# Kernel optimization log

Hardware: AMD Instinct MI355X
Metric: run time of the kernel (lower is better)

## Reference

```python
import jax, jax.numpy as jnp
from jax import lax
import numpy as np

# TopoLoss(dim=1, p=2, topo_lambda=1.0)
# p=2 -> Euclidean ground metric for the Vietoris-Rips filtration.
# This reference computes the dominant H0 persistence diagram of the VR complex:
# for a point cloud, H0 births are all 0 and deaths are exactly the MST edge
# weights (Kruskal/union-find == Prim, computed here with a fixed-length scan).
# Wasserstein distance between the two diagrams (equal cardinality N-1, births 0)
# reduces to optimal 1D matching of the sorted death values (q=1, the
# torch_topological WassersteinDistance default).
TOPO_LAMBDA = 1.0
EPS = 1e-12


def _pairwise_euclidean(x):
    # x: [B, N, D] -> [B, N, N] via the Gram trick (avoids [B,N,N,D] temp)
    sq = jnp.sum(x * x, axis=-1)                      # [B, N]
    g = jnp.einsum('bnd,bmd->bnm', x, x)              # [B, N, N]
    d2 = sq[:, :, None] + sq[:, None, :] - 2.0 * g
    return jnp.sqrt(jnp.maximum(d2, 0.0) + EPS)


def _mst_deaths(D):
    # Prim's algorithm on a dense distance matrix D: [N, N].
    # Returns the sorted MST edge weights = H0 death times ([N-1]).
    N = D.shape[0]
    inf = jnp.asarray(jnp.inf, D.dtype)
    in_tree0 = jnp.zeros((N,), bool).at[0].set(True)
    min_dist0 = D[0]

    def step(carry, _):
        in_tree, min_dist = carry
        masked = jnp.where(in_tree, inf, min_dist)
        j = jnp.argmin(masked)
        death = masked[j]
        in_tree = in_tree.at[j].set(True)
        min_dist = jnp.minimum(min_dist, D[j])
        return (in_tree, min_dist), death

    _, deaths = lax.scan(step, (in_tree0, min_dist0), None, length=N - 1)
    return jnp.sort(deaths)


def _h0_diagram_deaths(x):
    # x: [B, N, D] -> sorted death values [B, N-1]
    D = _pairwise_euclidean(x)
    return jax.vmap(_mst_deaths)(D)


def setup_inputs() -> dict:
    key = jax.random.key(0)
    k1, k2 = jax.random.split(key)
    B, N, D = 64, 1024, 3
    gts = jax.random.normal(k1, (B, N, D), dtype=jnp.float32)
    preds = jax.random.normal(k2, (B, N, D), dtype=jnp.float32)
    return {"gts": gts, "preds": preds}


def reference(gts, preds):
    # note: source names pers_info_pred = complex(gts) (vars swapped there);
    # Wasserstein is symmetric so ordering is irrelevant.
    deaths_a = _h0_diagram_deaths(gts)    # [B, N-1]
    deaths_b = _h0_diagram_deaths(preds)  # [B, N-1]
    # W1 between diagrams with equal cardinality and births==0:
    # optimal matching of sorted death coordinates.
    per_batch = jnp.sum(jnp.abs(deaths_a - deaths_b), axis=-1)  # [B]
    return per_batch.mean() * TOPO_LAMBDA
```

## Files before the change

### kernel.cpp

```cpp
#include <hip/hip_runtime.h>
#include <math.h>

#define N 1024
#define T 1024
#define HALF 512
#define PHASE_CAP 10
#define SWITCH 160

typedef float v2f __attribute__((ext_vector_type(2)));
typedef unsigned long long ull;

#define INF64 0xFFFFFFFFFFFFFFFFull
#define INF32 0xFFFFFFFFu

__device__ __forceinline__ unsigned umin32(unsigned a, unsigned b) { return a < b ? a : b; }
__device__ __forceinline__ unsigned umax32(unsigned a, unsigned b) { return a > b ? a : b; }
__device__ __forceinline__ int imin32(int a, int b) { return a < b ? a : b; }

__device__ __forceinline__ unsigned walk_root(const unsigned* parent, unsigned x) {
    unsigned prev = x, cur = parent[x];
    while (cur != prev) {
        unsigned nxt = parent[cur];
        if (nxt == prev) { cur = umin32(cur, prev); break; }
        prev = cur; cur = nxt;
    }
    return cur;
}

#define DPP_MIN_SHR(v, sh)                                                                   \
    do {                                                                                     \
        unsigned _t = (unsigned)__builtin_amdgcn_update_dpp(                                 \
            (int)0xFFFFFFFF, (int)(v), 0x110 | (sh), 0xF, 0xF, false);                       \
        (v) = umin32((v), _t);                                                               \
    } while (0)

__global__ __launch_bounds__(T) void scan1_kernel(const float* __restrict__ gts,
                                                  const float* __restrict__ preds,
                                                  unsigned* __restrict__ bests1) {
    __shared__ float px[N], py[N], pz[N];
    __shared__ float stage[3 * N];
    __shared__ unsigned pb[2][HALF];
    const int t = threadIdx.x;
    const int cloud = blockIdx.x >> 1;
    const int nh = blockIdx.x & 1;
    const float* __restrict__ src = (cloud < 64 ? gts : preds) + (size_t)(cloud & 63) * N * 3;

    if (t < 768) ((float4*)stage)[t] = ((const float4*)src)[t];
    __syncthreads();
    px[t] = stage[3 * t]; py[t] = stage[3 * t + 1]; pz[t] = stage[3 * t + 2];
    __syncthreads();

    const int node = nh * HALF + (t & (HALF - 1));
    const int jb = (t >> 9) * HALF;
    const float ax = px[node], ay = py[node], az = pz[node];
    const v2f axv = (v2f){ax, ax}, ayv = (v2f){ay, ay}, azv = (v2f){az, az};
    unsigned best = INF32;
    #pragma unroll 8
    for (int jj = 0; jj < HALF; jj += 2) {
        int j = jb + jj;
        v2f qx = *(const v2f*)&px[j];
        v2f qy = *(const v2f*)&py[j];
        v2f qz = *(const v2f*)&pz[j];
        v2f dx = axv - qx, dy = ayv - qy, dz = azv - qz;
        v2f e = dx * dx;
        e = __builtin_elementwise_fma(dy, dy, e);
        e = __builtin_elementwise_fma(dz, dz, e);
        unsigned k0 = (__float_as_uint(e.x) & 0xFFFFF800u) | (unsigned)j;
        unsigned k1 = (__float_as_uint(e.y) & 0xFFFFF800u) | (unsigned)(j + 1);
        k0 = (j == node) ? INF32 : k0;
        k1 = (j + 1 == node) ? INF32 : k1;
        best = umin32(best, umin32(k0, k1));
    }
    pb[t >> 9][t & (HALF - 1)] = best;
    __syncthreads();
    if (t < HALF)
        bests1[(size_t)cloud * N + nh * HALF + t] = umin32(pb[0][t], pb[1][t]);
}

__global__ __launch_bounds__(T) void scan2_kernel(const float* __restrict__ gts,
                                                  const float* __restrict__ preds,
                                                  const unsigned* __restrict__ bests1,
                                                  unsigned* __restrict__ bests2) {
    __shared__ float px[N], py[N], pz[N];
    __shared__ float stage[3 * N];
    __shared__ unsigned cw[N];
    __shared__ unsigned parent[N];
    __shared__ unsigned pb[2][HALF];
    const int t = threadIdx.x;
    const int cloud = blockIdx.x >> 1;
    const int nh = blockIdx.x & 1;
    const float* __restrict__ src = (cloud < 64 ? gts : preds) + (size_t)(cloud & 63) * N * 3;

    if (t < 768) ((float4*)stage)[t] = ((const float4*)src)[t];
    __syncthreads();
    px[t] = stage[3 * t]; py[t] = stage[3 * t + 1]; pz[t] = stage[3 * t + 2];
    parent[t] = bests1[(size_t)cloud * N + t] & 0x3FFu;
    __syncthreads();
    {
        unsigned r = walk_root(parent, (unsigned)t);
        parent[t] = r;
        cw[t] = r;
    }
    __syncthreads();

    const int node = nh * HALF + (t & (HALF - 1));
    const int jb = (t >> 9) * HALF;
    const unsigned c0 = cw[node];
    const float ax = px[node], ay = py[node], az = pz[node];
    const v2f axv = (v2f){ax, ax}, ayv = (v2f){ay, ay}, azv = (v2f){az, az};
    unsigned best = INF32;
    #pragma unroll 8
    for (int jj = 0; jj < HALF; jj += 2) {
        int j = jb + jj;
        v2f qx = *(const v2f*)&px[j];
        v2f qy = *(const v2f*)&py[j];
        v2f qz = *(const v2f*)&pz[j];
        uint2 cj = *(const uint2*)&cw[j];
        v2f dx = axv - qx, dy = ayv - qy, dz = azv - qz;
        v2f e = dx * dx;
        e = __builtin_elementwise_fma(dy, dy, e);
        e = __builtin_elementwise_fma(dz, dz, e);
        unsigned k0 = (__float_as_uint(e.x) & 0xFFFFF800u) | (unsigned)j;
        unsigned k1 = (__float_as_uint(e.y) & 0xFFFFF800u) | (unsigned)(j + 1);
        k0 = (cj.x == c0) ? INF32 : k0;
        k1 = (cj.y == c0) ? INF32 : k1;
        best = umin32(best, umin32(k0, k1));
    }
    pb[t >> 9][t & (HALF - 1)] = best;
    __syncthreads();
    if (t < HALF)
        bests2[(size_t)cloud * N + nh * HALF + t] = umin32(pb[0][t], pb[1][t]);
}

__global__ __launch_bounds__(T) void final_kernel(const float* __restrict__ gts,
                                                  const float* __restrict__ preds,
                                                  float* __restrict__ ws,
                                                  const unsigned* __restrict__ bests1,
                                                  const unsigned* __restrict__ bests2,
                                                  int nPre) {
    __shared__ float4 pts[N];
    __shared__ float4 spts[N];
    __shared__ unsigned comp[N];
    __shared__ ull bestComp[N];
    __shared__ unsigned parent[N];
    __shared__ __align__(16) unsigned pb[2][N];
    __shared__ float deaths[N];
    __shared__ int deathCount;

    const int t = threadIdx.x;
    const int blk = blockIdx.x;
    const float* __restrict__ src = (blk < 64 ? gts : preds) + (size_t)(blk & 63) * N * 3;

    {
        float* stg = (float*)&spts[0];
        if (t < 768) ((float4*)stg)[t] = ((const float4*)src)[t];
        __syncthreads();
        float x = stg[3 * t], y = stg[3 * t + 1], z = stg[3 * t + 2];
        pts[t] = make_float4(x, y, z, __uint_as_float((unsigned)t));
        comp[t] = (unsigned)t;
        parent[t] = (unsigned)t;
        deaths[t] = 0.0f;
        bestComp[t] = INF64;
    }
    if (t == 0) deathCount = 0;
    __syncthreads();

    const int n = t & (HALF - 1);
    const int h = t >> 9;
    const int n2 = n + HALF;
    const int jbase = h * HALF;
    float4 pA = pts[n], pB = pts[n2];
    const v2f pxv = (v2f){pA.x, pB.x};
    const v2f pyv = (v2f){pA.y, pB.y};
    const v2f pzv = (v2f){pA.z, pB.z};

    if (nPre >= 1) {
        unsigned b1 = bests1[(size_t)blk * N + t];
        unsigned j1 = b1 & 0x3FFu;
        unsigned e1 = b1 & 0xFFFFF800u;
        parent[t] = j1;
        __syncthreads();
        {
            unsigned p = j1;
            unsigned gp = parent[p];
            bool mutual = (gp == (unsigned)t);
            bool rec = !mutual || ((unsigned)t < p);
            float dval = rec ? sqrtf(__uint_as_float(e1) + 1e-12f) : 0.0f;
            ull m = __ballot(rec);
            int cnt = __popcll(m);
            int base = 0;
            if ((t & 63) == 0 && cnt) base = atomicAdd(&deathCount, cnt);
            base = __shfl(base, 0, 64);
            if (rec) {
                int idx = base + __popcll(m & ((1ull << (t & 63)) - 1ull));
                if (idx < N - 1) deaths[idx] = dval;
            }
        }
        __syncthreads();
        {
            unsigned r = walk_root(parent, (unsigned)t);
            parent[t] = r;
            comp[t] = r;
            pts[t].w = __uint_as_float(r);
        }
        __syncthreads();
    }

    if (nPre >= 2) {
        unsigned b2 = bests2[(size_t)blk * N + t];
        if (b2 != INF32) {
            unsigned j2 = b2 & 0x3FFu, e2 = b2 & 0xFFFFF800u;
            unsigned mn = umin32((unsigned)t, j2), mx = umax32((unsigned)t, j2);
            atomicMin(&bestComp[comp[t]], ((ull)e2 << 20) | (ull)((mn << 10) | mx));
        }
        __syncthreads();
        const unsigned c = (unsigned)t;
        const bool isRoot = (parent[c] == c);
        {
            ull bc = bestComp[c];
            if (isRoot && bc != INF64) {
                unsigned mn = (unsigned)((bc >> 10) & 0x3FFu);
                unsigned mx = (unsigned)(bc & 0x3FFu);
                unsigned cm = comp[mn];
                parent[c] = (cm == c) ? comp[mx] : cm;
            }
        }
        __syncthreads();
        {
            bool rec = false;
            float dval = 0.0f;
            unsigned p = parent[c];
            if (isRoot && p != c) {
                unsigned gp = parent[p];
                bool mutual = (gp == c);
                rec = !mutual || (c < p);
                if (rec) dval = sqrtf(__uint_as_float((unsigned)(bestComp[c] >> 20)) + 1e-12f);
            }
            ull m = __ballot(rec);
            int cnt = __popcll(m);
            int base = 0;
            if ((t & 63) == 0 && cnt) base = atomicAdd(&deathCount, cnt);
            base = __shfl(base, 0, 64);
            if (rec) {
                int idx = base + __popcll(m & ((1ull << (t & 63)) - 1ull));
                if (idx < N - 1) deaths[idx] = dval;
            }
        }
        __syncthreads();
        {
            unsigned r = walk_root(parent, c);
            parent[t] = r;
            unsigned nc = walk_root(parent, comp[t]);
            comp[t] = nc;
            pts[t].w = __uint_as_float(nc);
            bestComp[t] = INF64;
        }
        __syncthreads();
    }

    int phase = nPre;
    while (N - deathCount > SWITCH && phase < PHASE_CAP) {
        const unsigned c0 = comp[n], c1 = comp[n2];
        unsigned best0 = INF32, best1 = INF32;
        #pragma unroll 8
        for (int jj = 0; jj < HALF; ++jj) {
            int j = jbase + jj;
            float4 pj = pts[j];
            unsigned cj = __float_as_uint(pj.w);
            v2f dx = pxv - (v2f){pj.x, pj.x};
            v2f dy = pyv - (v2f){pj.y, pj.y};
            v2f dz = pzv - (v2f){pj.z, pj.z};
            v2f e = dx * dx;
            e = __builtin_elementwise_fma(dy, dy, e);
            e = __builtin_elementwise_fma(dz, dz, e);
            unsigned k0 = (__float_as_uint(e.x) & 0xFFFFF800u) | (unsigned)j;
            unsigned k1 = (__float_as_uint(e.y) & 0xFFFFF800u) | (unsigned)j;
            k0 = (cj == c0) ? INF32 : k0;
            k1 = (cj == c1) ? INF32 : k1;
            best0 = umin32(best0, k0);
            best1 = umin32(best1, k1);
        }
        pb[h][n] = best0;
        pb[h][n2] = best1;
        __syncthreads();
        if (h == 0) {
            #pragma unroll
            for (int s = 0; s < 2; ++s) {
                int m = s == 0 ? n : n2;
                unsigned fb = umin32(pb[0][m], pb[1][m]);
                if (fb != INF32) {
                    unsigned j = fb & 0x3FFu, e = fb & 0xFFFFF800u;
                    unsigned mn = umin32((unsigned)m, j), mx = umax32((unsigned)m, j);
                    ull key = ((ull)e << 20) | (ull)((mn << 10) | mx);
                    if (phase == 0) bestComp[m] = key;
                    else atomicMin(&bestComp[comp[m]], key);
                }
            }
        }
        __syncthreads();
        const unsigned c = (unsigned)t;
        const bool isRoot = (parent[c] == c);
        {
            ull bc = bestComp[c];
            if (isRoot && bc != INF64) {
                unsigned mn = (unsigned)((bc >> 10) & 0x3FFu);
                unsigned mx = (unsigned)(bc & 0x3FFu);
                unsigned cm = comp[mn];
                parent[c] = (cm == c) ? comp[mx] : cm;
            }
        }
        __syncthreads();
        {
            bool rec = false;
            float dval = 0.0f;
            unsigned p = parent[c];
            if (isRoot && p != c) {
                unsigned gp = parent[p];
                bool mutual = (gp == c);
                rec = !mutual || (c < p);
                if (rec) dval = sqrtf(__uint_as_float((unsigned)(bestComp[c] >> 20)) + 1e-12f);
            }
            ull m = __ballot(rec);
            int cnt = __popcll(m);
            int base = 0;
            if ((t & 63) == 0 && cnt) base = atomicAdd(&deathCount, cnt);
            base = __shfl(base, 0, 64);
            if (rec) {
                int idx = base + __popcll(m & ((1ull << (t & 63)) - 1ull));
                if (idx < N - 1) deaths[idx] = dval;
            }
        }
        __syncthreads();
        {
            unsigned r = walk_root(parent, c);
            parent[t] = r;
            unsigned nc = walk_root(parent, comp[t]);
            comp[t] = nc;
            pts[t].w = __uint_as_float(nc);
            bestComp[t] = INF64;
        }
        __syncthreads();
        ++phase;
    }

    const int dcbase = deathCount;
    const int comps = N - dcbase;
    if (comps > 1) {
        unsigned* sk = &pb[0][0];
        unsigned* wavemin = &pb[1][0];
        uint2* segs = (uint2*)&bestComp[0];
        sk[t] = (comp[t] << 10) | (unsigned)t;
        __syncthreads();
        for (int k = 2; k <= N; k <<= 1) {
            for (int j = k >> 1; j > 0; j >>= 1) {
                int ixj = t ^ j;
                if (ixj > t) {
                    unsigned a = sk[t], cc = sk[ixj];
                    bool up = ((t & k) == 0);
                    if ((a > cc) == up) { sk[t] = cc; sk[ixj] = a; }
                }
                __syncthreads();
            }
        }
        {
            unsigned key = sk[t];
            unsigned cme = key >> 10;
            spts[t] = pts[key & 0x3FFu];
            if (t == 0 || (sk[t - 1] >> 10) != cme) segs[cme].x = (unsigned)t;
            if (t == N - 1 || (sk[t + 1] >> 10) != cme) segs[cme].y = (unsigned)t + 1;
        }
        __syncthreads();

        const int lane = t & 63;
        const int wid = t >> 6;
        unsigned c_cur = comp[0];
        v2f pxv2 = (v2f){0.f, 0.f}, pyv2 = pxv2, pzv2 = pxv2;
        unsigned myc0 = 0, myc1 = 0, md0 = INF32, md1 = INF32;
        if (t < HALF) {
            float4 q0 = spts[t], q1 = spts[t + HALF];
            myc0 = sk[t] >> 10;
            myc1 = sk[t + HALF] >> 10;
            pxv2 = (v2f){q0.x, q1.x};
            pyv2 = (v2f){q0.y, q1.y};
            pzv2 = (v2f){q0.z, q1.z};
            if (myc0 == c_cur) pxv2.x = INFINITY;
            if (myc1 == c_cur) pxv2.y = INFINITY;
        }

        for (int step = 0; step < comps - 1; ++step) {
            if (t < HALF) {
                uint2 sg = segs[c_cur];
                const int jb = (int)sg.x, je = (int)sg.y, jl = je - 1;
                for (int base = jb; base < je; base += 4) {
                    float4 q0 = spts[base];
                    float4 q1 = spts[imin32(base + 1, jl)];
                    float4 q2 = spts[imin32(base + 2, jl)];
                    float4 q3 = spts[imin32(base + 3, jl)];
                    #define RELAX(qq)                                                        \
                        {                                                                    \
                            v2f dx = pxv2 - (v2f){qq.x, qq.x};                               \
                            v2f dy = pyv2 - (v2f){qq.y, qq.y};                               \
                            v2f dz = pzv2 - (v2f){qq.z, qq.z};                               \
                            v2f e = dx * dx;                                                 \
                            e = __builtin_elementwise_fma(dy, dy, e);                        \
                            e = __builtin_elementwise_fma(dz, dz, e);                        \
                            md0 = umin32(md0, (__float_as_uint(e.x) & 0xFFFFFC00u) | myc0);  \
                            md1 = umin32(md1, (__float_as_uint(e.y) & 0xFFFFFC00u) | myc1);  \
                        }
                    RELAX(q0) RELAX(q1) RELAX(q2) RELAX(q3)
                    #undef RELAX
                }
                unsigned v = umin32(md0, md1);
                DPP_MIN_SHR(v, 1);
                DPP_MIN_SHR(v, 2);
                DPP_MIN_SHR(v, 4);
                DPP_MIN_SHR(v, 8);
                unsigned r0 = (unsigned)__builtin_amdgcn_readlane((int)v, 15);
                unsigned r1 = (unsigned)__builtin_amdgcn_readlane((int)v, 31);
                unsigned r2 = (unsigned)__builtin_amdgcn_readlane((int)v, 47);
                unsigned r3 = (unsigned)__builtin_amdgcn_readlane((int)v, 63);
                if (lane == 0)
                    wavemin[(step & 1) * 8 + wid] = umin32(umin32(r0, r1), umin32(r2, r3));
            }
            __syncthreads();
            if (t < HALF) {
                const uint4* wmv = (const uint4*)(wavemin + (step & 1) * 8);
                uint4 u0 = wmv[0], u1 = wmv[1];
                unsigned m0 = umin32(umin32(u0.x, u0.y), umin32(u0.z, u0.w));
                unsigned m1 = umin32(umin32(u1.x, u1.y), umin32(u1.z, u1.w));
                unsigned G = umin32(m0, m1);
                c_cur = G & 0x3FFu;
                if (t == 0)
                    deaths[dcbase + step] = sqrtf(__uint_as_float(G & 0xFFFFFC00u) + 1e-12f);
                if (myc0 == c_cur) { pxv2.x = INFINITY; md0 = INF32; }
                if (myc1 == c_cur) { pxv2.y = INFINITY; md1 = INF32; }
            }
        }
    }

    if (t == 0) deaths[N - 1] = INFINITY;
    __syncthreads();
    for (int k = 2; k <= N; k <<= 1) {
        for (int j = k >> 1; j > 0; j >>= 1) {
            int ixj = t ^ j;
            if (ixj > t) {
                float a = deaths[t], cc = deaths[ixj];
                bool up = ((t & k) == 0);
                if ((a > cc) == up) { deaths[t] = cc; deaths[ixj] = a; }
            }
            __syncthreads();
        }
    }

    float* dst = ws + (size_t)blk * N;
    dst[t] = (t < N - 1) ? deaths[t] : 0.0f;
}

__global__ __launch_bounds__(256) void diff_kernel(const float* __restrict__ ws,
                                                   float* __restrict__ out) {
    __shared__ float red[4];
    const int t = threadIdx.x;
    const int b = blockIdx.x;
    const float* a = ws + (size_t)b * N;
    const float* c = ws + (size_t)(64 + b) * N;
    float sum = 0.0f;
    for (int i = t; i < N; i += 256)
        sum += fabsf(a[i] - c[i]);
    #pragma unroll
    for (int off = 32; off > 0; off >>= 1)
        sum += __shfl_down(sum, off, 64);
    if ((t & 63) == 0) red[t >> 6] = sum;
    __syncthreads();
    if (t == 0)
        atomicAdd(out, (red[0] + red[1] + red[2] + red[3]) * (1.0f / 64.0f));
}

extern "C" void kernel_launch(void* const* d_in, const int* in_sizes, int n_in,
                              void* d_out, int out_size, void* d_ws, size_t ws_size,
                              hipStream_t stream) {
    const float* gts = (const float*)d_in[0];
    const float* preds = (const float*)d_in[1];
    float* ws = (float*)d_ws;
    unsigned* bests1 = (unsigned*)d_ws;
    unsigned* bests2 = bests1 + 128 * N;
    const bool big = ws_size >= (size_t)(2u * 128u * N * 4u);

    if (big) {
        hipLaunchKernelGGL(scan1_kernel, dim3(256), dim3(T), 0, stream, gts, preds, bests1);
        hipLaunchKernelGGL(scan2_kernel, dim3(256), dim3(T), 0, stream, gts, preds, bests1, bests2);
        hipLaunchKernelGGL(final_kernel, dim3(128), dim3(T), 0, stream,
                           gts, preds, ws, bests1, bests2, 2);
    } else {
        hipLaunchKernelGGL(final_kernel, dim3(128), dim3(T), 0, stream,
                           gts, preds, ws, (const unsigned*)nullptr, (const unsigned*)nullptr, 0);
    }
    hipMemsetAsync(d_out, 0, sizeof(float), stream);
    hipLaunchKernelGGL(diff_kernel, dim3(64), dim3(256), 0, stream, ws, (float*)d_out);
}
```

Measured before the change: 233.4 us.

## Add third Boruvka prepass kernel to offload another phase from final kernel

Adds a scan3 kernel that rebuilds the component labels after phases one and two, then computes each node's nearest out-of-component neighbour over 256 blocks (two per cloud). The final kernel now loops over the precomputed phases, consuming bests3 as a third Boruvka merge step, which leaves fewer components for its own single-block-per-cloud search. It only runs when the workspace holds three buffers. In exchange it adds an extra kernel launch, a redundant recomputation of the earlier merges, and more global traffic.

```diff
diff --git a/kernel.cpp b/kernel.cpp
--- a/kernel.cpp
+++ b/kernel.cpp
@@ -132,11 +132,92 @@
         bests2[(size_t)cloud * N + nh * HALF + t] = umin32(pb[0][t], pb[1][t]);
 }
 
+__global__ __launch_bounds__(T) void scan3_kernel(const float* __restrict__ gts,
+                                                  const float* __restrict__ preds,
+                                                  const unsigned* __restrict__ bests1,
+                                                  const unsigned* __restrict__ bests2,
+                                                  unsigned* __restrict__ bests3) {
+    __shared__ float px[N], py[N], pz[N];
+    __shared__ float stage[3 * N];
+    __shared__ unsigned cw[N];
+    __shared__ unsigned parent[N];
+    __shared__ ull bestC[N];
+    __shared__ unsigned pb[2][HALF];
+    const int t = threadIdx.x;
+    const int cloud = blockIdx.x >> 1;
+    const int nh = blockIdx.x & 1;
+    const float* __restrict__ src = (cloud < 64 ? gts : preds) + (size_t)(cloud & 63) * N * 3;
+
+    if (t < 768) ((float4*)stage)[t] = ((const float4*)src)[t];
+    __syncthreads();
+    px[t] = stage[3 * t]; py[t] = stage[3 * t + 1]; pz[t] = stage[3 * t + 2];
+    parent[t] = bests1[(size_t)cloud * N + t] & 0x3FFu;
+    bestC[t] = INF64;
+    __syncthreads();
+    {
+        unsigned r = walk_root(parent, (unsigned)t);
+        parent[t] = r;
+        cw[t] = r;
+    }
+    __syncthreads();
+    {
+        unsigned b2 = bests2[(size_t)cloud * N + t];
+        if (b2 != INF32) {
+            unsigned j2 = b2 & 0x3FFu, e2 = b2 & 0xFFFFF800u;
+            unsigned mn = umin32((unsigned)t, j2), mx = umax32((unsigned)t, j2);
+            atomicMin(&bestC[cw[t]], ((ull)e2 << 20) | (ull)((mn << 10) | mx));
+        }
+    }
+    __syncthreads();
+    {
+        const unsigned c = (unsigned)t;
+        ull bc = bestC[c];
+        if (parent[c] == c && bc != INF64) {
+            unsigned mn = (unsigned)((bc >> 10) & 0x3FFu);
+            unsigned mx = (unsigned)(bc & 0x3FFu);
+            unsigned cm = cw[mn];
+            parent[c] = (cm == c) ? cw[mx] : cm;
+        }
+    }
+    __syncthreads();
+    cw[t] = walk_root(parent, cw[t]);
+    __syncthreads();
+
+    const int node = nh * HALF + (t & (HALF - 1));
+    const int jb = (t >> 9) * HALF;
+    const unsigned c0 = cw[node];
+    const float ax = px[node], ay = py[node], az = pz[node];
+    const v2f axv = (v2f){ax, ax}, ayv = (v2f){ay, ay}, azv = (v2f){az, az};
+    unsigned best = INF32;
+    #pragma unroll 8
+    for (int jj = 0; jj < HALF; jj += 2) {
+        int j = jb + jj;
+        v2f qx = *(const v2f*)&px[j];
+        v2f qy = *(const v2f*)&py[j];
+        v2f qz = *(const v2f*)&pz[j];
+        uint2 cj = *(const uint2*)&cw[j];
+        v2f dx = axv - qx, dy = ayv - qy, dz = azv - qz;
+        v2f e = dx * dx;
+        e = __builtin_elementwise_fma(dy, dy, e);
+        e = __builtin_elementwise_fma(dz, dz, e);
+        unsigned k0 = (__float_as_uint(e.x) & 0xFFFFF800u) | (unsigned)j;
+        unsigned k1 = (__float_as_uint(e.y) & 0xFFFFF800u) | (unsigned)(j + 1);
+        k0 = (cj.x == c0) ? INF32 : k0;
+        k1 = (cj.y == c0) ? INF32 : k1;
+        best = umin32(best, umin32(k0, k1));
+    }
+    pb[t >> 9][t & (HALF - 1)] = best;
+    __syncthreads();
+    if (t < HALF)
+        bests3[(size_t)cloud * N + nh * HALF + t] = umin32(pb[0][t], pb[1][t]);
+}
+
 __global__ __launch_bounds__(T) void final_kernel(const float* __restrict__ gts,
                                                   const float* __restrict__ preds,
                                                   float* __restrict__ ws,
                                                   const unsigned* __restrict__ bests1,
                                                   const unsigned* __restrict__ bests2,
+                                                  const unsigned* __restrict__ bests3,
                                                   int nPre) {
     __shared__ float4 pts[N];
     __shared__ float4 spts[N];
@@ -206,8 +287,9 @@
         __syncthreads();
     }
 
-    if (nPre >= 2) {
-        unsigned b2 = bests2[(size_t)blk * N + t];
+    for (int ph = 2; ph <= nPre; ++ph) {
+        const unsigned* __restrict__ bsrc = (ph == 2) ? bests2 : bests3;
+        unsigned b2 = bsrc[(size_t)blk * N + t];
         if (b2 != INF32) {
             unsigned j2 = b2 & 0x3FFu, e2 = b2 & 0xFFFFF800u;
             unsigned mn = umin32((unsigned)t, j2), mx = umax32((unsigned)t, j2);
@@ -483,16 +565,22 @@
     float* ws = (float*)d_ws;
     unsigned* bests1 = (unsigned*)d_ws;
     unsigned* bests2 = bests1 + 128 * N;
-    const bool big = ws_size >= (size_t)(2u * 128u * N * 4u);
-
-    if (big) {
+    unsigned* bests3 = bests2 + 128 * N;
+    const size_t SEG = (size_t)128 * N * 4;
+    const int nPre = (ws_size >= 3 * SEG) ? 3 : (ws_size >= 2 * SEG ? 2 : 0);
+
+    if (nPre >= 2) {
         hipLaunchKernelGGL(scan1_kernel, dim3(256), dim3(T), 0, stream, gts, preds, bests1);
         hipLaunchKernelGGL(scan2_kernel, dim3(256), dim3(T), 0, stream, gts, preds, bests1, bests2);
+        if (nPre == 3)
+            hipLaunchKernelGGL(scan3_kernel, dim3(256), dim3(T), 0, stream,
+                               gts, preds, bests1, bests2, bests3);
         hipLaunchKernelGGL(final_kernel, dim3(128), dim3(T), 0, stream,
-                           gts, preds, ws, bests1, bests2, 2);
+                           gts, preds, ws, bests1, bests2, bests3, nPre);
     } else {
         hipLaunchKernelGGL(final_kernel, dim3(128), dim3(T), 0, stream,
-                           gts, preds, ws, (const unsigned*)nullptr, (const unsigned*)nullptr, 0);
+                           gts, preds, ws, (const unsigned*)nullptr, (const unsigned*)nullptr,
+                           (const unsigned*)nullptr, 0);
     }
     hipMemsetAsync(d_out, 0, sizeof(float), stream);
     hipLaunchKernelGGL(diff_kernel, dim3(64), dim3(256), 0, stream, ws, (float*)d_out);
```

Result: slower. 242.6 us (+4.0%).

## Fuse scan, Boruvka and diff stages into one cooperative mega kernel

Applied to the files above, without the earlier changes.

Replaces the separate scan1, scan2, final and diff launches with a single cooperative kernel of 256 blocks that uses grid.sync between stages. It also adds a third parallel nearest-other-component scan across all 256 blocks, so the 128-block final stage begins with fewer components. The goal is to cut launch gaps and move more of the Boruvka work into the fully parallel phase. In exchange it relies on all 256 blocks of 1024 threads being co-resident, pays for grid-wide barriers, and leaves half the grid idle during the final stage. If the cooperative launch fails, it falls back to the unfused final and diff kernels.

```diff
diff --git a/kernel.cpp b/kernel.cpp
--- a/kernel.cpp
+++ b/kernel.cpp
@@ -1,5 +1,8 @@
 #include <hip/hip_runtime.h>
+#include <hip/hip_cooperative_groups.h>
 #include <math.h>
+
+namespace cg = cooperative_groups;
 
 #define N 1024
 #define T 1024
@@ -34,79 +37,12 @@
         (v) = umin32((v), _t);                                                               \
     } while (0)
 
-__global__ __launch_bounds__(T) void scan1_kernel(const float* __restrict__ gts,
-                                                  const float* __restrict__ preds,
-                                                  unsigned* __restrict__ bests1) {
-    __shared__ float px[N], py[N], pz[N];
-    __shared__ float stage[3 * N];
-    __shared__ unsigned pb[2][HALF];
-    const int t = threadIdx.x;
-    const int cloud = blockIdx.x >> 1;
-    const int nh = blockIdx.x & 1;
-    const float* __restrict__ src = (cloud < 64 ? gts : preds) + (size_t)(cloud & 63) * N * 3;
-
-    if (t < 768) ((float4*)stage)[t] = ((const float4*)src)[t];
-    __syncthreads();
-    px[t] = stage[3 * t]; py[t] = stage[3 * t + 1]; pz[t] = stage[3 * t + 2];
-    __syncthreads();
-
-    const int node = nh * HALF + (t & (HALF - 1));
-    const int jb = (t >> 9) * HALF;
-    const float ax = px[node], ay = py[node], az = pz[node];
-    const v2f axv = (v2f){ax, ax}, ayv = (v2f){ay, ay}, azv = (v2f){az, az};
-    unsigned best = INF32;
-    #pragma unroll 8
-    for (int jj = 0; jj < HALF; jj += 2) {
-        int j = jb + jj;
-        v2f qx = *(const v2f*)&px[j];
-        v2f qy = *(const v2f*)&py[j];
-        v2f qz = *(const v2f*)&pz[j];
-        v2f dx = axv - qx, dy = ayv - qy, dz = azv - qz;
-        v2f e = dx * dx;
-        e = __builtin_elementwise_fma(dy, dy, e);
-        e = __builtin_elementwise_fma(dz, dz, e);
-        unsigned k0 = (__float_as_uint(e.x) & 0xFFFFF800u) | (unsigned)j;
-        unsigned k1 = (__float_as_uint(e.y) & 0xFFFFF800u) | (unsigned)(j + 1);
-        k0 = (j == node) ? INF32 : k0;
-        k1 = (j + 1 == node) ? INF32 : k1;
-        best = umin32(best, umin32(k0, k1));
-    }
-    pb[t >> 9][t & (HALF - 1)] = best;
-    __syncthreads();
-    if (t < HALF)
-        bests1[(size_t)cloud * N + nh * HALF + t] = umin32(pb[0][t], pb[1][t]);
-}
-
-__global__ __launch_bounds__(T) void scan2_kernel(const float* __restrict__ gts,
-                                                  const float* __restrict__ preds,
-                                                  const unsigned* __restrict__ bests1,
-                                                  unsigned* __restrict__ bests2) {
-    __shared__ float px[N], py[N], pz[N];
-    __shared__ float stage[3 * N];
-    __shared__ unsigned cw[N];
-    __shared__ unsigned parent[N];
-    __shared__ unsigned pb[2][HALF];
-    const int t = threadIdx.x;
-    const int cloud = blockIdx.x >> 1;
-    const int nh = blockIdx.x & 1;
-    const float* __restrict__ src = (cloud < 64 ? gts : preds) + (size_t)(cloud & 63) * N * 3;
-
-    if (t < 768) ((float4*)stage)[t] = ((const float4*)src)[t];
-    __syncthreads();
-    px[t] = stage[3 * t]; py[t] = stage[3 * t + 1]; pz[t] = stage[3 * t + 2];
-    parent[t] = bests1[(size_t)cloud * N + t] & 0x3FFu;
-    __syncthreads();
-    {
-        unsigned r = walk_root(parent, (unsigned)t);
-        parent[t] = r;
-        cw[t] = r;
-    }
-    __syncthreads();
-
-    const int node = nh * HALF + (t & (HALF - 1));
-    const int jb = (t >> 9) * HALF;
-    const unsigned c0 = cw[node];
-    const float ax = px[node], ay = py[node], az = pz[node];
+__device__ __forceinline__ unsigned scan_half(const float* __restrict__ px,
+                                              const float* __restrict__ py,
+                                              const float* __restrict__ pz,
+                                              const unsigned* __restrict__ cw,
+                                              unsigned c0, float ax, float ay, float az,
+                                              int jb) {
     const v2f axv = (v2f){ax, ax}, ayv = (v2f){ay, ay}, azv = (v2f){az, az};
     unsigned best = INF32;
     #pragma unroll 8
@@ -126,18 +62,436 @@
         k1 = (cj.y == c0) ? INF32 : k1;
         best = umin32(best, umin32(k0, k1));
     }
-    pb[t >> 9][t & (HALF - 1)] = best;
-    __syncthreads();
-    if (t < HALF)
-        bests2[(size_t)cloud * N + nh * HALF + t] = umin32(pb[0][t], pb[1][t]);
+    return best;
+}
+
+__global__ __launch_bounds__(T) void mega_kernel(const float* __restrict__ gts,
+                                                 const float* __restrict__ preds,
+                                                 float* __restrict__ ws,
+                                                 unsigned* __restrict__ bests1,
+                                                 unsigned* __restrict__ bests2,
+                                                 unsigned* __restrict__ bests3,
+                                                 float* __restrict__ out) {
+    cg::grid_group grid = cg::this_grid();
+    __shared__ float4 pts[N];
+    __shared__ float4 spts[N];
+    __shared__ __align__(16) unsigned comp[N];
+    __shared__ ull bestComp[N];
+    __shared__ unsigned parent[N];
+    __shared__ __align__(16) unsigned pb[2][N];
+    __shared__ float deaths[N];
+    __shared__ int deathCount;
+
+    const int t = threadIdx.x;
+    const int blk = blockIdx.x;
+
+    {
+        const int cloud = blk >> 1;
+        const int nh = blk & 1;
+        const float* __restrict__ src =
+            (cloud < 64 ? gts : preds) + (size_t)(cloud & 63) * N * 3;
+        float* px = (float*)&spts[0];
+        float* py = px + N;
+        float* pz = py + N;
+        float* stage = (float*)&pts[0];
+
+        if (t < 768) ((float4*)stage)[t] = ((const float4*)src)[t];
+        __syncthreads();
+        px[t] = stage[3 * t]; py[t] = stage[3 * t + 1]; pz[t] = stage[3 * t + 2];
+        comp[t] = (unsigned)t;
+        __syncthreads();
+
+        const int node = nh * HALF + (t & (HALF - 1));
+        const int jb = (t >> 9) * HALF;
+        const float ax = px[node], ay = py[node], az = pz[node];
+
+        pb[0][t] = scan_half(px, py, pz, comp, comp[node], ax, ay, az, jb);
+        __syncthreads();
+        if (t < HALF)
+            bests1[(size_t)cloud * N + nh * HALF + t] = umin32(pb[0][t], pb[0][t + HALF]);
+        grid.sync();
+
+        parent[t] = bests1[(size_t)cloud * N + t] & 0x3FFu;
+        __syncthreads();
+        {
+            unsigned r = walk_root(parent, (unsigned)t);
+            parent[t] = r;
+            comp[t] = r;
+        }
+        __syncthreads();
+
+        pb[0][t] = scan_half(px, py, pz, comp, comp[node], ax, ay, az, jb);
+        __syncthreads();
+        if (t < HALF)
+            bests2[(size_t)cloud * N + nh * HALF + t] = umin32(pb[0][t], pb[0][t + HALF]);
+        grid.sync();
+
+        bestComp[t] = INF64;
+        __syncthreads();
+        {
+            unsigned b2 = bests2[(size_t)cloud * N + t];
+            if (b2 != INF32) {
+                unsigned j2 = b2 & 0x3FFu, e2 = b2 & 0xFFFFF800u;
+                unsigned mn = umin32((unsigned)t, j2), mx = umax32((unsigned)t, j2);
+                atomicMin(&bestComp[comp[t]], ((ull)e2 << 20) | (ull)((mn << 10) | mx));
+            }
+        }
+        __syncthreads();
+        {
+            const unsigned c = (unsigned)t;
+            ull bc = bestComp[c];
+            if (parent[c] == c && bc != INF64) {
+                unsigned mn = (unsigned)((bc >> 10) & 0x3FFu);
+                unsigned mx = (unsigned)(bc & 0x3FFu);
+                unsigned cm = comp[mn];
+                parent[c] = (cm == c) ? comp[mx] : cm;
+            }
+        }
+        __syncthreads();
+        comp[t] = walk_root(parent, comp[t]);
+        __syncthreads();
+
+        pb[0][t] = scan_half(px, py, pz, comp, comp[node], ax, ay, az, jb);
+        __syncthreads();
+        if (t < HALF)
+            bests3[(size_t)cloud * N + nh * HALF + t] = umin32(pb[0][t], pb[0][t + HALF]);
+    }
+    grid.sync();
+
+    if (blk < 128) {
+        const float* __restrict__ src =
+            (blk < 64 ? gts : preds) + (size_t)(blk & 63) * N * 3;
+        {
+            float* stg = (float*)&spts[0];
+            if (t < 768) ((float4*)stg)[t] = ((const float4*)src)[t];
+            __syncthreads();
+            float x = stg[3 * t], y = stg[3 * t + 1], z = stg[3 * t + 2];
+            pts[t] = make_float4(x, y, z, __uint_as_float((unsigned)t));
+            comp[t] = (unsigned)t;
+            parent[t] = (unsigned)t;
+            deaths[t] = 0.0f;
+            bestComp[t] = INF64;
+        }
+        if (t == 0) deathCount = 0;
+        __syncthreads();
+
+        const int n = t & (HALF - 1);
+        const int h = t >> 9;
+        const int n2 = n + HALF;
+        const int jbase = h * HALF;
+        float4 pA = pts[n], pB = pts[n2];
+        const v2f pxv = (v2f){pA.x, pB.x};
+        const v2f pyv = (v2f){pA.y, pB.y};
+        const v2f pzv = (v2f){pA.z, pB.z};
+
+        {
+            unsigned b1 = bests1[(size_t)blk * N + t];
+            unsigned j1 = b1 & 0x3FFu;
+            unsigned e1 = b1 & 0xFFFFF800u;
+            parent[t] = j1;
+            __syncthreads();
+            {
+                unsigned p = j1;
+                unsigned gp = parent[p];
+                bool mutual = (gp == (unsigned)t);
+                bool rec = !mutual || ((unsigned)t < p);
+                float dval = rec ? sqrtf(__uint_as_float(e1) + 1e-12f) : 0.0f;
+                ull m = __ballot(rec);
+                int cnt = __popcll(m);
+                int base = 0;
+                if ((t & 63) == 0 && cnt) base = atomicAdd(&deathCount, cnt);
+                base = __shfl(base, 0, 64);
+                if (rec) {
+                    int idx = base + __popcll(m & ((1ull << (t & 63)) - 1ull));
+                    if (idx < N - 1) deaths[idx] = dval;
+                }
+            }
+            __syncthreads();
+            {
+                unsigned r = walk_root(parent, (unsigned)t);
+                parent[t] = r;
+                comp[t] = r;
+                pts[t].w = __uint_as_float(r);
+            }
+            __syncthreads();
+        }
+
+        for (int ph = 2; ph <= 3; ++ph) {
+            const unsigned* __restrict__ bsrc = (ph == 2) ? bests2 : bests3;
+            unsigned b2 = bsrc[(size_t)blk * N + t];
+            if (b2 != INF32) {
+                unsigned j2 = b2 & 0x3FFu, e2 = b2 & 0xFFFFF800u;
+                unsigned mn = umin32((unsigned)t, j2), mx = umax32((unsigned)t, j2);
+                atomicMin(&bestComp[comp[t]], ((ull)e2 << 20) | (ull)((mn << 10) | mx));
+            }
+            __syncthreads();
+            const unsigned c = (unsigned)t;
+            const bool isRoot = (parent[c] == c);
+            {
+                ull bc = bestComp[c];
+                if (isRoot && bc != INF64) {
+                    unsigned mn = (unsigned)((bc >> 10) & 0x3FFu);
+                    unsigned mx = (unsigned)(bc & 0x3FFu);
+                    unsigned cm = comp[mn];
+                    parent[c] = (cm == c) ? comp[mx] : cm;
+                }
+            }
+            __syncthreads();
+            {
+                bool rec = false;
+                float dval = 0.0f;
+                unsigned p = parent[c];
+                if (isRoot && p != c) {
+                    unsigned gp = parent[p];
+                    bool mutual = (gp == c);
+                    rec = !mutual || (c < p);
+                    if (rec)
+                        dval = sqrtf(__uint_as_float((unsigned)(bestComp[c] >> 20)) + 1e-12f);
+                }
+                ull m = __ballot(rec);
+                int cnt = __popcll(m);
+                int base = 0;
+                if ((t & 63) == 0 && cnt) base = atomicAdd(&deathCount, cnt);
+                base = __shfl(base, 0, 64);
+                if (rec) {
+                    int idx = base + __popcll(m & ((1ull << (t & 63)) - 1ull));
+                    if (idx < N - 1) deaths[idx] = dval;
+                }
+            }
+            __syncthreads();
+            {
+                unsigned r = walk_root(parent, c);
+                parent[t] = r;
+                unsigned nc = walk_root(parent, comp[t]);
+                comp[t] = nc;
+                pts[t].w = __uint_as_float(nc);
+                bestComp[t] = INF64;
+            }
+            __syncthreads();
+        }
+
+        int phase = 3;
+        while (N - deathCount > SWITCH && phase < PHASE_CAP) {
+            const unsigned c0 = comp[n], c1 = comp[n2];
+            unsigned best0 = INF32, best1 = INF32;
+            #pragma unroll 8
+            for (int jj = 0; jj < HALF; ++jj) {
+                int j = jbase + jj;
+                float4 pj = pts[j];
+                unsigned cj = __float_as_uint(pj.w);
+                v2f dx = pxv - (v2f){pj.x, pj.x};
+                v2f dy = pyv - (v2f){pj.y, pj.y};
+                v2f dz = pzv - (v2f){pj.z, pj.z};
+                v2f e = dx * dx;
+                e = __builtin_elementwise_fma(dy, dy, e);
+                e = __builtin_elementwise_fma(dz, dz, e);
+                unsigned k0 = (__float_as_uint(e.x) & 0xFFFFF800u) | (unsigned)j;
+                unsigned k1 = (__float_as_uint(e.y) & 0xFFFFF800u) | (unsigned)j;
+                k0 = (cj == c0) ? INF32 : k0;
+                k1 = (cj == c1) ? INF32 : k1;
+                best0 = umin32(best0, k0);
+                best1 = umin32(best1, k1);
+            }
+            pb[h][n] = best0;
+            pb[h][n2] = best1;
+            __syncthreads();
+            if (h == 0) {
+                #pragma unroll
+                for (int s = 0; s < 2; ++s) {
+                    int m = s == 0 ? n : n2;
+                    unsigned fb = umin32(pb[0][m], pb[1][m]);
+                    if (fb != INF32) {
+                        unsigned j = fb & 0x3FFu, e = fb & 0xFFFFF800u;
+                        unsigned mn = umin32((unsigned)m, j), mx = umax32((unsigned)m, j);
+                        atomicMin(&bestComp[comp[m]], ((ull)e << 20) | (ull)((mn << 10) | mx));
+                    }
+                }
+            }
+            __syncthreads();
+            const unsigned c = (unsigned)t;
+            const bool isRoot = (parent[c] == c);
+            {
+                ull bc = bestComp[c];
+                if (isRoot && bc != INF64) {
+                    unsigned mn = (unsigned)((bc >> 10) & 0x3FFu);
+                    unsigned mx = (unsigned)(bc & 0x3FFu);
+                    unsigned cm = comp[mn];
+                    parent[c] = (cm == c) ? comp[mx] : cm;
+                }
+            }
+            __syncthreads();
+            {
+                bool rec = false;
+                float dval = 0.0f;
+                unsigned p = parent[c];
+                if (isRoot && p != c) {
+                    unsigned gp = parent[p];
+                    bool mutual = (gp == c);
+                    rec = !mutual || (c < p);
+                    if (rec)
+                        dval = sqrtf(__uint_as_float((unsigned)(bestComp[c] >> 20)) + 1e-12f);
+                }
+                ull m = __ballot(rec);
+                int cnt = __popcll(m);
+                int base = 0;
+                if ((t & 63) == 0 && cnt) base = atomicAdd(&deathCount, cnt);
+                base = __shfl(base, 0, 64);
+                if (rec) {
+                    int idx = base + __popcll(m & ((1ull << (t & 63)) - 1ull));
+                    if (idx < N - 1) deaths[idx] = dval;
+                }
+            }
+            __syncthreads();
+            {
+                unsigned r = walk_root(parent, c);
+                parent[t] = r;
+                unsigned nc = walk_root(parent, comp[t]);
+                comp[t] = nc;
+                pts[t].w = __uint_as_float(nc);
+                bestComp[t] = INF64;
+            }
+            __syncthreads();
+            ++phase;
+        }
+
+        const int dcbase = deathCount;
+        const int comps = N - dcbase;
+        if (comps > 1) {
+            unsigned* sk = &pb[0][0];
+            unsigned* wavemin = &pb[1][0];
+            uint2* segs = (uint2*)&bestComp[0];
+            sk[t] = (comp[t] << 10) | (unsigned)t;
+            __syncthreads();
+            for (int k = 2; k <= N; k <<= 1) {
+                for (int j = k >> 1; j > 0; j >>= 1) {
+                    int ixj = t ^ j;
+                    if (ixj > t) {
+                        unsigned a = sk[t], cc = sk[ixj];
+                        bool up = ((t & k) == 0);
+                        if ((a > cc) == up) { sk[t] = cc; sk[ixj] = a; }
+                    }
+                    __syncthreads();
+                }
+            }
+            {
+                unsigned key = sk[t];
+                unsigned cme = key >> 10;
+                spts[t] = pts[key & 0x3FFu];
+                if (t == 0 || (sk[t - 1] >> 10) != cme) segs[cme].x = (unsigned)t;
+                if (t == N - 1 || (sk[t + 1] >> 10) != cme) segs[cme].y = (unsigned)t + 1;
+            }
+            __syncthreads();
+
+            const int lane = t & 63;
+            const int wid = t >> 6;
+            unsigned c_cur = comp[0];
+            v2f pxv2 = (v2f){0.f, 0.f}, pyv2 = pxv2, pzv2 = pxv2;
+            unsigned myc0 = 0, myc1 = 0, md0 = INF32, md1 = INF32;
+            if (t < HALF) {
+                float4 q0 = spts[t], q1 = spts[t + HALF];
+                myc0 = sk[t] >> 10;
+                myc1 = sk[t + HALF] >> 10;
+                pxv2 = (v2f){q0.x, q1.x};
+                pyv2 = (v2f){q0.y, q1.y};
+                pzv2 = (v2f){q0.z, q1.z};
+                if (myc0 == c_cur) pxv2.x = INFINITY;
+                if (myc1 == c_cur) pxv2.y = INFINITY;
+            }
+
+            for (int step = 0; step < comps - 1; ++step) {
+                if (t < HALF) {
+                    uint2 sg = segs[c_cur];
+                    const int jb2 = (int)sg.x, je = (int)sg.y, jl = je - 1;
+                    for (int base = jb2; base < je; base += 4) {
+                        float4 q0 = spts[base];
+                        float4 q1 = spts[imin32(base + 1, jl)];
+                        float4 q2 = spts[imin32(base + 2, jl)];
+                        float4 q3 = spts[imin32(base + 3, jl)];
+                        #define RELAX(qq)                                                    \
+                            {                                                                \
+                                v2f dx = pxv2 - (v2f){qq.x, qq.x};                           \
+                                v2f dy = pyv2 - (v2f){qq.y, qq.y};                           \
+                                v2f dz = pzv2 - (v2f){qq.z, qq.z};                           \
+                                v2f e = dx * dx;                                             \
+                                e = __builtin_elementwise_fma(dy, dy, e);                    \
+                                e = __builtin_elementwise_fma(dz, dz, e);                    \
+                                md0 = umin32(md0,                                            \
+                                    (__float_as_uint(e.x) & 0xFFFFFC00u) | myc0);            \
+                                md1 = umin32(md1,                                            \
+                                    (__float_as_uint(e.y) & 0xFFFFFC00u) | myc1);            \
+                            }
+                        RELAX(q0) RELAX(q1) RELAX(q2) RELAX(q3)
+                        #undef RELAX
+                    }
+                    unsigned v = umin32(md0, md1);
+                    DPP_MIN_SHR(v, 1);
+                    DPP_MIN_SHR(v, 2);
+                    DPP_MIN_SHR(v, 4);
+                    DPP_MIN_SHR(v, 8);
+                    unsigned r0 = (unsigned)__builtin_amdgcn_readlane((int)v, 15);
+                    unsigned r1 = (unsigned)__builtin_amdgcn_readlane((int)v, 31);
+                    unsigned r2 = (unsigned)__builtin_amdgcn_readlane((int)v, 47);
+                    unsigned r3 = (unsigned)__builtin_amdgcn_readlane((int)v, 63);
+                    if (lane == 0)
+                        wavemin[(step & 1) * 8 + wid] =
+                            umin32(umin32(r0, r1), umin32(r2, r3));
+                }
+                __syncthreads();
+                if (t < HALF) {
+                    const uint4* wmv = (const uint4*)(wavemin + (step & 1) * 8);
+                    uint4 u0 = wmv[0], u1 = wmv[1];
+                    unsigned m0 = umin32(umin32(u0.x, u0.y), umin32(u0.z, u0.w));
+                    unsigned m1 = umin32(umin32(u1.x, u1.y), umin32(u1.z, u1.w));
+                    unsigned G = umin32(m0, m1);
+                    c_cur = G & 0x3FFu;
+                    if (t == 0)
+                        deaths[dcbase + step] =
+                            sqrtf(__uint_as_float(G & 0xFFFFFC00u) + 1e-12f);
+                    if (myc0 == c_cur) { pxv2.x = INFINITY; md0 = INF32; }
+                    if (myc1 == c_cur) { pxv2.y = INFINITY; md1 = INF32; }
+                }
+            }
+        }
+
+        if (t == 0) deaths[N - 1] = INFINITY;
+        __syncthreads();
+        for (int k = 2; k <= N; k <<= 1) {
+            for (int j = k >> 1; j > 0; j >>= 1) {
+                int ixj = t ^ j;
+                if (ixj > t) {
+                    float a = deaths[t], cc = deaths[ixj];
+                    bool up = ((t & k) == 0);
+                    if ((a > cc) == up) { deaths[t] = cc; deaths[ixj] = a; }
+                }
+                __syncthreads();
+            }
+        }
+
+        float* dst = ws + (size_t)blk * N;
+        dst[t] = (t < N - 1) ? deaths[t] : 0.0f;
+    }
+    grid.sync();
+
+    if (blk < 64) {
+        float sum = fabsf(ws[(size_t)blk * N + t] - ws[(size_t)(64 + blk) * N + t]);
+        #pragma unroll
+        for (int off = 32; off > 0; off >>= 1)
+            sum += __shfl_down(sum, off, 64);
+        float* redf = (float*)&pb[0][0];
+        if ((t & 63) == 0) redf[t >> 6] = sum;
+        __syncthreads();
+        if (t == 0) {
+            float tot = 0.0f;
+            #pragma unroll
+            for (int k = 0; k < 16; ++k) tot += redf[k];
+            atomicAdd(out, tot * (1.0f / 64.0f));
+        }
+    }
 }
 
 __global__ __launch_bounds__(T) void final_kernel(const float* __restrict__ gts,
                                                   const float* __restrict__ preds,
-                                                  float* __restrict__ ws,
-                                                  const unsigned* __restrict__ bests1,
-                                                  const unsigned* __restrict__ bests2,
-                                                  int nPre) {
+                                                  float* __restrict__ ws) {
     __shared__ float4 pts[N];
     __shared__ float4 spts[N];
     __shared__ unsigned comp[N];
@@ -174,91 +528,7 @@
     const v2f pyv = (v2f){pA.y, pB.y};
     const v2f pzv = (v2f){pA.z, pB.z};
 
-    if (nPre >= 1) {
-        unsigned b1 = bests1[(size_t)blk * N + t];
-        unsigned j1 = b1 & 0x3FFu;
-        unsigned e1 = b1 & 0xFFFFF800u;
-        parent[t] = j1;
-        __syncthreads();
-        {
-            unsigned p = j1;
-            unsigned gp = parent[p];
-            bool mutual = (gp == (unsigned)t);
-            bool rec = !mutual || ((unsigned)t < p);
-            float dval = rec ? sqrtf(__uint_as_float(e1) + 1e-12f) : 0.0f;
-            ull m = __ballot(rec);
-            int cnt = __popcll(m);
-            int base = 0;
-            if ((t & 63) == 0 && cnt) base = atomicAdd(&deathCount, cnt);
-            base = __shfl(base, 0, 64);
-            if (rec) {
-                int idx = base + __popcll(m & ((1ull << (t & 63)) - 1ull));
-                if (idx < N - 1) deaths[idx] = dval;
-            }
-        }
-        __syncthreads();
-        {
-            unsigned r = walk_root(parent, (unsigned)t);
-            parent[t] = r;
-            comp[t] = r;
-            pts[t].w = __uint_as_float(r);
-        }
-        __syncthreads();
-    }
-
-    if (nPre >= 2) {
-        unsigned b2 = bests2[(size_t)blk * N + t];
-        if (b2 != INF32) {
-            unsigned j2 = b2 & 0x3FFu, e2 = b2 & 0xFFFFF800u;
-            unsigned mn = umin32((unsigned)t, j2), mx = umax32((unsigned)t, j2);
-            atomicMin(&bestComp[comp[t]], ((ull)e2 << 20) | (ull)((mn << 10) | mx));
-        }
-        __syncthreads();
-        const unsigned c = (unsigned)t;
-        const bool isRoot = (parent[c] == c);
-        {
-            ull bc = bestComp[c];
-            if (isRoot && bc != INF64) {
-                unsigned mn = (unsigned)((bc >> 10) & 0x3FFu);
-                unsigned mx = (unsigned)(bc & 0x3FFu);
-                unsigned cm = comp[mn];
-                parent[c] = (cm == c) ? comp[mx] : cm;
-            }
-        }
-        __syncthreads();
-        {
-            bool rec = false;
-            float dval = 0.0f;
-            unsigned p = parent[c];
-            if (isRoot && p != c) {
-                unsigned gp = parent[p];
-                bool mutual = (gp == c);
-                rec = !mutual || (c < p);
-                if (rec) dval = sqrtf(__uint_as_float((unsigned)(bestComp[c] >> 20)) + 1e-12f);
-            }
-            ull m = __ballot(rec);
-            int cnt = __popcll(m);
-            int base = 0;
-            if ((t & 63) == 0 && cnt) base = atomicAdd(&deathCount, cnt);
-            base = __shfl(base, 0, 64);
-            if (rec) {
-                int idx = base + __popcll(m & ((1ull << (t & 63)) - 1ull));
-                if (idx < N - 1) deaths[idx] = dval;
-            }
-        }
-        __syncthreads();
-        {
-            unsigned r = walk_root(parent, c);
-            parent[t] = r;
-            unsigned nc = walk_root(parent, comp[t]);
-            comp[t] = nc;
-            pts[t].w = __uint_as_float(nc);
-            bestComp[t] = INF64;
-        }
-        __syncthreads();
-    }
-
-    int phase = nPre;
+    int phase = 0;
     while (N - deathCount > SWITCH && phase < PHASE_CAP) {
         const unsigned c0 = comp[n], c1 = comp[n2];
         unsigned best0 = INF32, best1 = INF32;
@@ -386,12 +656,11 @@
             if (myc0 == c_cur) pxv2.x = INFINITY;
             if (myc1 == c_cur) pxv2.y = INFINITY;
         }
-
         for (int step = 0; step < comps - 1; ++step) {
             if (t < HALF) {
                 uint2 sg = segs[c_cur];
-                const int jb = (int)sg.x, je = (int)sg.y, jl = je - 1;
-                for (int base = jb; base < je; base += 4) {
+                const int jb2 = (int)sg.x, je = (int)sg.y, jl = je - 1;
+                for (int base = jb2; base < je; base += 4) {
                     float4 q0 = spts[base];
                     float4 q1 = spts[imin32(base + 1, jl)];
                     float4 q2 = spts[imin32(base + 2, jl)];
@@ -483,17 +752,22 @@
     float* ws = (float*)d_ws;
     unsigned* bests1 = (unsigned*)d_ws;
     unsigned* bests2 = bests1 + 128 * N;
-    const bool big = ws_size >= (size_t)(2u * 128u * N * 4u);
-
-    if (big) {
-        hipLaunchKernelGGL(scan1_kernel, dim3(256), dim3(T), 0, stream, gts, preds, bests1);
-        hipLaunchKernelGGL(scan2_kernel, dim3(256), dim3(T), 0, stream, gts, preds, bests1, bests2);
-        hipLaunchKernelGGL(final_kernel, dim3(128), dim3(T), 0, stream,
-                           gts, preds, ws, bests1, bests2, 2);
-    } else {
-        hipLaunchKernelGGL(final_kernel, dim3(128), dim3(T), 0, stream,
-                           gts, preds, ws, (const unsigned*)nullptr, (const unsigned*)nullptr, 0);
-    }
+    unsigned* bests3 = bests2 + 128 * N;
+    float* outp = (float*)d_out;
+    const size_t SEG = (size_t)128 * N * 4;
+
     hipMemsetAsync(d_out, 0, sizeof(float), stream);
-    hipLaunchKernelGGL(diff_kernel, dim3(64), dim3(256), 0, stream, ws, (float*)d_out);
+
+    bool ok = false;
+    if (ws_size >= 3 * SEG) {
+        void* args[] = {(void*)&gts, (void*)&preds, (void*)&ws,
+                        (void*)&bests1, (void*)&bests2, (void*)&bests3, (void*)&outp};
+        hipError_t err = hipLaunchCooperativeKernel((const void*)mega_kernel,
+                                                    dim3(256), dim3(T), args, 0, stream);
+        ok = (err == hipSuccess);
+    }
+    if (!ok) {
+        hipLaunchKernelGGL(final_kernel, dim3(128), dim3(T), 0, stream, gts, preds, ws);
+        hipLaunchKernelGGL(diff_kernel, dim3(64), dim3(256), 0, stream, ws, outp);
+    }
 }
```

Result: slower. 357.1 us (+53.0%).
